# Kernel optimization log

Hardware: AMD Instinct MI355X
Metric: run time of the kernel (lower is better)

The kernel has to match this reference:

```python
import jax, jax.numpy as jnp
import numpy as np
from jax import lax

K = 3           # dynamic-filter kernel size
NUM_TYPES = 216 # Qstr*Qcohe*Qangle = 3*3*24
C = 64          # in/out channels
GROUP = 4


def _conv(x, w, groups=1):
    return lax.conv_general_dilated(
        x, w, window_strides=(1, 1), padding='SAME',
        dimension_numbers=('NCHW', 'OIHW', 'NCHW'),
        feature_group_count=groups)


def setup_inputs() -> dict:
    key = jax.random.key(0)
    ks = jax.random.split(key, 7)
    B, H, W = 1, 64, 64
    x = jax.random.normal(ks[0], (B, C, H, W), dtype=jnp.float32)
    buckets = jax.random.randint(ks[1], (B, H, W), 0, NUM_TYPES)
    # body1: grouped 3x3 conv (in=out=64, groups=4 -> in/group=16)
    w1 = jax.random.normal(ks[2], (C, C // GROUP, 3, 3), dtype=jnp.float32) * 0.05
    b1 = jax.random.normal(ks[3], (C,), dtype=jnp.float32) * 0.05
    # filter embedding: one flattened (out, in*K*K + bias) filter per bucket type
    emb = jax.random.normal(ks[4], (NUM_TYPES, C * (C * K * K + 1)), dtype=jnp.float32) * 0.1
    # body2: 1x1 conv
    w2 = jax.random.normal(ks[5], (C, C, 1, 1), dtype=jnp.float32) * 0.05
    b2 = jax.random.normal(ks[6], (C,), dtype=jnp.float32) * 0.05
    return {'x': x, 'buckets': buckets, 'w1': w1, 'b1': b1, 'emb': emb, 'w2': w2, 'b2': b2}


def reference(x, buckets, w1, b1, emb, w2, b2):
    B, Cin, H, W = x.shape
    Cout = w2.shape[0]
    ckk = emb.shape[1] // Cout - 1  # in*K*K
    # body1: grouped conv + ReLU
    h = jax.nn.relu(_conv(x, w1, groups=GROUP) + b1[None, :, None, None])
    # per-pixel bucket-indexed dynamic conv
    patches = lax.conv_general_dilated_patches(
        h, (K, K), (1, 1), 'SAME',
        dimension_numbers=('NCHW', 'OIHW', 'NCHW'))  # [B, Cin*K*K, H, W]
    f = emb[buckets].reshape(B, H, W, Cout, ckk + 1)   # gathered per-pixel filters
    out = jnp.einsum('bchw,bhwoc->bohw', patches, f[..., :-1])
    out = out + jnp.transpose(f[..., -1], (0, 3, 1, 2))  # per-pixel bias
    # body2: ReLU -> 1x1 conv
    out = _conv(jax.nn.relu(out), w2) + b2[None, :, None, None]
    # residual + ReLU
    return jax.nn.relu(out + x)
```

## Files before the change

kernel.cpp:

```cpp
#include <hip/hip_runtime.h>

#define NTYPES 216
#define NPIX   4096
#define KD     576
#define ROWLEN 577
#define NPC    32
#define PSTR   640

typedef __attribute__((ext_vector_type(8))) short short8;
typedef __attribute__((ext_vector_type(4))) float f32x4;
typedef __attribute__((ext_vector_type(4), aligned(4))) float f32x4u;
typedef __attribute__((ext_vector_type(8))) unsigned short u16x8;
typedef __attribute__((ext_vector_type(4))) unsigned short u16x4;

static __device__ __forceinline__ unsigned short f2bf(float f) {
    unsigned u = __builtin_bit_cast(unsigned, f);
    unsigned r = (u + 0x7FFFu + ((u >> 16) & 1u)) >> 16;
    return (unsigned short)r;
}

__global__ __launch_bounds__(256) void prep_kernel(
        const float* __restrict__ x, const float* __restrict__ w1,
        const float* __restrict__ b1, const int* __restrict__ buckets,
        unsigned short* __restrict__ hbf, int* __restrict__ offsets,
        int* __restrict__ sorted) {
    int tid = threadIdx.x;
    if (blockIdx.x == 256) {
        __shared__ int cnt[256];
        __shared__ int pre[256];
        cnt[tid] = 0;
        __syncthreads();
        for (int i = tid; i < NPIX; i += 256) atomicAdd(&cnt[buckets[i]], 1);
        __syncthreads();
        int v = cnt[tid];
        pre[tid] = v;
        __syncthreads();
        #pragma unroll
        for (int s = 1; s < 256; s <<= 1) {
            int add = (tid >= s) ? pre[tid - s] : 0;
            __syncthreads();
            pre[tid] += add;
            __syncthreads();
        }
        int excl = pre[tid] - v;
        if (tid <= NTYPES) offsets[tid] = excl;
        cnt[tid] = excl;
        __syncthreads();
        for (int i = tid; i < NPIX; i += 256) {
            int b = buckets[i];
            sorted[atomicAdd(&cnt[b], 1)] = i;
        }
        return;
    }
    int flat = blockIdx.x * 256 + tid;
    int x4 = flat & 15;
    int y  = (flat >> 4) & 63;
    int c  = flat >> 10;
    int g  = c >> 4;
    const float* wrow = w1 + c * 144;
    float o0, o1, o2, o3;
    o0 = o1 = o2 = o3 = b1[c];
    #pragma unroll
    for (int ci = 0; ci < 16; ++ci) {
        const float* xp = x + (g * 16 + ci) * 4096;
        #pragma unroll
        for (int dy = 0; dy < 3; ++dy) {
            int yy = y + dy - 1;
            if (yy < 0 || yy > 63) continue;
            const float* row = xp + yy * 64 + x4 * 4;
            f32x4 mm = *(const f32x4*)row;
            float xl = (x4 > 0)  ? row[-1] : 0.f;
            float xr = (x4 < 15) ? row[4]  : 0.f;
            float wa = wrow[ci * 9 + dy * 3 + 0];
            float wb = wrow[ci * 9 + dy * 3 + 1];
            float wc = wrow[ci * 9 + dy * 3 + 2];
            o0 = fmaf(wa, xl,    fmaf(wb, mm[0], fmaf(wc, mm[1], o0)));
            o1 = fmaf(wa, mm[0], fmaf(wb, mm[1], fmaf(wc, mm[2], o1)));
            o2 = fmaf(wa, mm[1], fmaf(wb, mm[2], fmaf(wc, mm[3], o2)));
            o3 = fmaf(wa, mm[2], fmaf(wb, mm[3], fmaf(wc, xr,    o3)));
        }
    }
    u16x4 r16;
    r16[0] = f2bf(fmaxf(o0, 0.f));
    r16[1] = f2bf(fmaxf(o1, 0.f));
    r16[2] = f2bf(fmaxf(o2, 0.f));
    r16[3] = f2bf(fmaxf(o3, 0.f));
    *(u16x4*)&hbf[flat * 4] = r16;
}

__global__ __launch_bounds__(512) void dyn_kernel(
        const unsigned short* __restrict__ hbf, const float* __restrict__ emb,
        const float* __restrict__ w2, const float* __restrict__ b2,
        const float* __restrict__ x, const int* __restrict__ offsets,
        const int* __restrict__ sorted, float* __restrict__ out) {

    __shared__ alignas(16) unsigned short Wl[64 * PSTR];
    __shared__ alignas(16) unsigned short Pl[NPC * PSTR];
    __shared__ alignas(16) unsigned short Dl[NPC * 72];
    __shared__ alignas(16) unsigned short w2l[64 * 72];
    __shared__ float bias_l[64];
    __shared__ int pixs[NPC];

    int t = blockIdx.x;
    int start = offsets[t];
    int n = offsets[t + 1] - start;
    if (n <= 0) return;

    int tid  = threadIdx.x;
    int lane = tid & 63;
    int wv   = tid >> 6;
    int m    = wv & 3;
    int ph   = wv >> 2;
    int ra   = lane & 15;
    int kg   = lane >> 4;

    const float* eb = emb + (size_t)t * 36928;

    #pragma unroll
    for (int it = 0; it < 9; ++it) {
        int u  = tid + it * 512;
        int r  = u / 72;
        int c0 = (u - r * 72) * 8;
        const float* src = eb + r * ROWLEN + c0;
        f32x4u a = *(const f32x4u*)src;
        f32x4u b = *(const f32x4u*)(src + 4);
        u16x8 v;
        #pragma unroll
        for (int j = 0; j < 4; ++j) { v[j] = f2bf(a[j]); v[j + 4] = f2bf(b[j]); }
        *(u16x8*)&Wl[r * PSTR + (r & 7) * 8 + c0] = v;
    }
    if (tid < 64) bias_l[tid] = eb[tid * ROWLEN + KD];

    {
        int o = tid >> 3, i8 = (tid & 7) * 8;
        const float* src = w2 + o * 64 + i8;
        u16x8 v;
        #pragma unroll
        for (int j = 0; j < 8; ++j) v[j] = f2bf(src[j]);
        *(u16x8*)&w2l[o * 72 + i8] = v;
    }
    __syncthreads();

    int rowW = m * 16 + ra;
    const unsigned short* pW = Wl + rowW * PSTR + (rowW & 7) * 8 + kg * 8;
    u16x8 Wr[9][2];
    #pragma unroll
    for (int ck = 0; ck < 9; ++ck) {
        Wr[ck][0] = *(const u16x8*)(pW + ck * 64);
        Wr[ck][1] = *(const u16x8*)(pW + ck * 64 + 32);
    }
    int ob0 = m * 16 + kg * 4;
    float bias0 = bias_l[ob0 + 0], bias1 = bias_l[ob0 + 1];
    float bias2 = bias_l[ob0 + 2], bias3 = bias_l[ob0 + 3];

    const unsigned short* pB = Pl + (ph * 16 + ra) * PSTR + (ra & 7) * 8 + kg * 8;

    int gp = tid >> 4;
    int gk = tid & 15;
    unsigned short* pdst = Pl + gp * PSTR + (gp & 7) * 8;

    for (int base = 0; base < n; base += NPC) {
        __syncthreads();
        if (tid < NPC) pixs[tid] = (base + tid < n) ? sorted[start + base + tid] : -1;
        __syncthreads();

        {
            int pixel = pixs[gp];
            int py = pixel >> 6, px = pixel & 63;
            #pragma unroll
            for (int pass = 0; pass < 9; ++pass) {
                int k0 = pass * 64 + gk * 4;
                u16x4 v;
                #pragma unroll
                for (int j = 0; j < 4; ++j) {
                    int k = k0 + j;
                    int cch = k / 9, r9 = k - cch * 9;
                    int dy = r9 / 3, dx = r9 - dy * 3;
                    unsigned short bits = 0;
                    if (pixel >= 0) {
                        int yy = py + dy - 1, xx = px + dx - 1;
                        if (yy >= 0 && yy < 64 && xx >= 0 && xx < 64)
                            bits = hbf[cch * 4096 + yy * 64 + xx];
                    }
                    v[j] = bits;
                }
                *(u16x4*)(pdst + k0) = v;
            }
        }
        __syncthreads();

        f32x4 acc = {0.f, 0.f, 0.f, 0.f};
        #pragma unroll
        for (int ck = 0; ck < 9; ++ck) {
            #pragma unroll
            for (int ks = 0; ks < 2; ++ks) {
                u16x8 bv = *(const u16x8*)(pB + ck * 64 + ks * 32);
                acc = __builtin_amdgcn_mfma_f32_16x16x32_bf16(
                          __builtin_bit_cast(short8, Wr[ck][ks]),
                          __builtin_bit_cast(short8, bv), acc, 0, 0, 0);
            }
        }

        {
            int pi = ph * 16 + ra;
            u16x4 dv;
            dv[0] = f2bf(fmaxf(acc[0] + bias0, 0.f));
            dv[1] = f2bf(fmaxf(acc[1] + bias1, 0.f));
            dv[2] = f2bf(fmaxf(acc[2] + bias2, 0.f));
            dv[3] = f2bf(fmaxf(acc[3] + bias3, 0.f));
            *(u16x4*)&Dl[pi * 72 + ob0] = dv;
        }
        __syncthreads();

        f32x4 acc2 = {0.f, 0.f, 0.f, 0.f};
        #pragma unroll
        for (int ks = 0; ks < 2; ++ks) {
            u16x8 a2  = *(const u16x8*)&w2l[(m * 16 + ra) * 72 + ks * 32 + kg * 8];
            u16x8 b2v = *(const u16x8*)&Dl[(ph * 16 + ra) * 72 + ks * 32 + kg * 8];
            acc2 = __builtin_amdgcn_mfma_f32_16x16x32_bf16(
                       __builtin_bit_cast(short8, a2),
                       __builtin_bit_cast(short8, b2v), acc2, 0, 0, 0);
        }

        {
            int pi = ph * 16 + ra;
            int pixel = pixs[pi];
            if (pixel >= 0) {
                #pragma unroll
                for (int j = 0; j < 4; ++j) {
                    int o = ob0 + j;
                    float v = acc2[j] + b2[o] + x[o * 4096 + pixel];
                    out[o * 4096 + pixel] = fmaxf(v, 0.f);
                }
            }
        }
    }
}

extern "C" void kernel_launch(void* const* d_in, const int* in_sizes, int n_in,
                              void* d_out, int out_size, void* d_ws, size_t ws_size,
                              hipStream_t stream) {
    const float* x       = (const float*)d_in[0];
    const int*   buckets = (const int*)d_in[1];
    const float* w1      = (const float*)d_in[2];
    const float* b1      = (const float*)d_in[3];
    const float* emb     = (const float*)d_in[4];
    const float* w2      = (const float*)d_in[5];
    const float* b2      = (const float*)d_in[6];
    float* out = (float*)d_out;

    char* ws = (char*)d_ws;
    unsigned short* hbf = (unsigned short*)ws;
    int*   offsets      = (int*)(ws + (1 << 20));
    int*   sorted       = (int*)(ws + (1 << 20) + 4096);

    prep_kernel<<<257, 256, 0, stream>>>(x, w1, b1, buckets, hbf, offsets, sorted);
    dyn_kernel<<<NTYPES, 512, 0, stream>>>(hbf, emb, w2, b2, x, offsets, sorted, out);
}
```

Before: 37.62 us.

## Fuse prep and dynamic-filter kernels into one cooperative launch with grid sync

The grouped-conv prep, the bucket sort and the dynamic per-bucket filter stage now run in a single cooperative kernel of 216 blocks, separated by a grid-wide sync. Each block issues its embedding-filter loads before doing prep work, so that global load latency overlaps the grouped conv and sort. This removes the second kernel launch and the gap between kernels. In exchange it adds cooperative-launch and grid-barrier overhead and puts more register pressure on the 512-thread prep path.

Result: slower. 114.6 us (+204.6%).

```diff
diff --git a/kernel.cpp b/kernel.cpp
--- a/kernel.cpp
+++ b/kernel.cpp
@@ -1,4 +1,7 @@
 #include <hip/hip_runtime.h>
+#include <hip/hip_cooperative_groups.h>
+
+namespace cg = cooperative_groups;
 
 #define NTYPES 216
 #define NPIX   4096
@@ -19,80 +22,13 @@
     return (unsigned short)r;
 }
 
-__global__ __launch_bounds__(256) void prep_kernel(
+__global__ __launch_bounds__(512) void fused_kernel(
         const float* __restrict__ x, const float* __restrict__ w1,
         const float* __restrict__ b1, const int* __restrict__ buckets,
+        const float* __restrict__ emb, const float* __restrict__ w2,
+        const float* __restrict__ b2,
         unsigned short* __restrict__ hbf, int* __restrict__ offsets,
-        int* __restrict__ sorted) {
-    int tid = threadIdx.x;
-    if (blockIdx.x == 256) {
-        __shared__ int cnt[256];
-        __shared__ int pre[256];
-        cnt[tid] = 0;
-        __syncthreads();
-        for (int i = tid; i < NPIX; i += 256) atomicAdd(&cnt[buckets[i]], 1);
-        __syncthreads();
-        int v = cnt[tid];
-        pre[tid] = v;
-        __syncthreads();
-        #pragma unroll
-        for (int s = 1; s < 256; s <<= 1) {
-            int add = (tid >= s) ? pre[tid - s] : 0;
-            __syncthreads();
-            pre[tid] += add;
-            __syncthreads();
-        }
-        int excl = pre[tid] - v;
-        if (tid <= NTYPES) offsets[tid] = excl;
-        cnt[tid] = excl;
-        __syncthreads();
-        for (int i = tid; i < NPIX; i += 256) {
-            int b = buckets[i];
-            sorted[atomicAdd(&cnt[b], 1)] = i;
-        }
-        return;
-    }
-    int flat = blockIdx.x * 256 + tid;
-    int x4 = flat & 15;
-    int y  = (flat >> 4) & 63;
-    int c  = flat >> 10;
-    int g  = c >> 4;
-    const float* wrow = w1 + c * 144;
-    float o0, o1, o2, o3;
-    o0 = o1 = o2 = o3 = b1[c];
-    #pragma unroll
-    for (int ci = 0; ci < 16; ++ci) {
-        const float* xp = x + (g * 16 + ci) * 4096;
-        #pragma unroll
-        for (int dy = 0; dy < 3; ++dy) {
-            int yy = y + dy - 1;
-            if (yy < 0 || yy > 63) continue;
-            const float* row = xp + yy * 64 + x4 * 4;
-            f32x4 mm = *(const f32x4*)row;
-            float xl = (x4 > 0)  ? row[-1] : 0.f;
-            float xr = (x4 < 15) ? row[4]  : 0.f;
-            float wa = wrow[ci * 9 + dy * 3 + 0];
-            float wb = wrow[ci * 9 + dy * 3 + 1];
-            float wc = wrow[ci * 9 + dy * 3 + 2];
-            o0 = fmaf(wa, xl,    fmaf(wb, mm[0], fmaf(wc, mm[1], o0)));
-            o1 = fmaf(wa, mm[0], fmaf(wb, mm[1], fmaf(wc, mm[2], o1)));
-            o2 = fmaf(wa, mm[1], fmaf(wb, mm[2], fmaf(wc, mm[3], o2)));
-            o3 = fmaf(wa, mm[2], fmaf(wb, mm[3], fmaf(wc, xr,    o3)));
-        }
-    }
-    u16x4 r16;
-    r16[0] = f2bf(fmaxf(o0, 0.f));
-    r16[1] = f2bf(fmaxf(o1, 0.f));
-    r16[2] = f2bf(fmaxf(o2, 0.f));
-    r16[3] = f2bf(fmaxf(o3, 0.f));
-    *(u16x4*)&hbf[flat * 4] = r16;
-}
-
-__global__ __launch_bounds__(512) void dyn_kernel(
-        const unsigned short* __restrict__ hbf, const float* __restrict__ emb,
-        const float* __restrict__ w2, const float* __restrict__ b2,
-        const float* __restrict__ x, const int* __restrict__ offsets,
-        const int* __restrict__ sorted, float* __restrict__ out) {
+        int* __restrict__ sorted, float* __restrict__ out) {
 
     __shared__ alignas(16) unsigned short Wl[64 * PSTR];
     __shared__ alignas(16) unsigned short Pl[NPC * PSTR];
@@ -100,137 +36,215 @@
     __shared__ alignas(16) unsigned short w2l[64 * 72];
     __shared__ float bias_l[64];
     __shared__ int pixs[NPC];
-
-    int t = blockIdx.x;
-    int start = offsets[t];
-    int n = offsets[t + 1] - start;
-    if (n <= 0) return;
-
-    int tid  = threadIdx.x;
-    int lane = tid & 63;
-    int wv   = tid >> 6;
-    int m    = wv & 3;
-    int ph   = wv >> 2;
-    int ra   = lane & 15;
-    int kg   = lane >> 4;
-
+    __shared__ int cnt[256];
+    __shared__ int pre[256];
+
+    int tid = threadIdx.x;
+    int t   = blockIdx.x;
     const float* eb = emb + (size_t)t * 36928;
 
+    f32x4u wa[9], wb[9];
     #pragma unroll
     for (int it = 0; it < 9; ++it) {
         int u  = tid + it * 512;
         int r  = u / 72;
         int c0 = (u - r * 72) * 8;
         const float* src = eb + r * ROWLEN + c0;
-        f32x4u a = *(const f32x4u*)src;
-        f32x4u b = *(const f32x4u*)(src + 4);
-        u16x8 v;
-        #pragma unroll
-        for (int j = 0; j < 4; ++j) { v[j] = f2bf(a[j]); v[j + 4] = f2bf(b[j]); }
-        *(u16x8*)&Wl[r * PSTR + (r & 7) * 8 + c0] = v;
-    }
-    if (tid < 64) bias_l[tid] = eb[tid * ROWLEN + KD];
+        wa[it] = *(const f32x4u*)src;
+        wb[it] = *(const f32x4u*)(src + 4);
+    }
+    float biasv = (tid < 64) ? eb[tid * ROWLEN + KD] : 0.f;
 
     {
         int o = tid >> 3, i8 = (tid & 7) * 8;
-        const float* src = w2 + o * 64 + i8;
+        const float* s2 = w2 + o * 64 + i8;
+        f32x4 q0 = *(const f32x4*)s2;
+        f32x4 q1 = *(const f32x4*)(s2 + 4);
         u16x8 v;
         #pragma unroll
-        for (int j = 0; j < 8; ++j) v[j] = f2bf(src[j]);
+        for (int j = 0; j < 4; ++j) { v[j] = f2bf(q0[j]); v[j + 4] = f2bf(q1[j]); }
         *(u16x8*)&w2l[o * 72 + i8] = v;
     }
-    __syncthreads();
-
-    int rowW = m * 16 + ra;
-    const unsigned short* pW = Wl + rowW * PSTR + (rowW & 7) * 8 + kg * 8;
-    u16x8 Wr[9][2];
+    if (tid < 64) bias_l[tid] = biasv;
+
+    if (blockIdx.x < 128) {
+        int flat = blockIdx.x * 512 + tid;
+        int x4 = flat & 15;
+        int y  = (flat >> 4) & 63;
+        int c  = flat >> 10;
+        int g  = c >> 4;
+        const float* wrow = w1 + c * 144;
+        float o0, o1, o2, o3;
+        o0 = o1 = o2 = o3 = b1[c];
+        #pragma unroll
+        for (int ci = 0; ci < 16; ++ci) {
+            const float* xp = x + (g * 16 + ci) * 4096;
+            #pragma unroll
+            for (int dy = 0; dy < 3; ++dy) {
+                int yy = y + dy - 1;
+                if (yy < 0 || yy > 63) continue;
+                const float* row = xp + yy * 64 + x4 * 4;
+                f32x4 mm = *(const f32x4*)row;
+                float xl = (x4 > 0)  ? row[-1] : 0.f;
+                float xr = (x4 < 15) ? row[4]  : 0.f;
+                float wwa = wrow[ci * 9 + dy * 3 + 0];
+                float wwb = wrow[ci * 9 + dy * 3 + 1];
+                float wwc = wrow[ci * 9 + dy * 3 + 2];
+                o0 = fmaf(wwa, xl,    fmaf(wwb, mm[0], fmaf(wwc, mm[1], o0)));
+                o1 = fmaf(wwa, mm[0], fmaf(wwb, mm[1], fmaf(wwc, mm[2], o1)));
+                o2 = fmaf(wwa, mm[1], fmaf(wwb, mm[2], fmaf(wwc, mm[3], o2)));
+                o3 = fmaf(wwa, mm[2], fmaf(wwb, mm[3], fmaf(wwc, xr,    o3)));
+            }
+        }
+        u16x4 r16;
+        r16[0] = f2bf(fmaxf(o0, 0.f));
+        r16[1] = f2bf(fmaxf(o1, 0.f));
+        r16[2] = f2bf(fmaxf(o2, 0.f));
+        r16[3] = f2bf(fmaxf(o3, 0.f));
+        *(u16x4*)&hbf[flat * 4] = r16;
+    } else if (blockIdx.x == 128) {
+        if (tid < 256) cnt[tid] = 0;
+        __syncthreads();
+        for (int i = tid; i < NPIX; i += 512) atomicAdd(&cnt[buckets[i]], 1);
+        __syncthreads();
+        int v = 0;
+        if (tid < 256) { v = cnt[tid]; pre[tid] = v; }
+        __syncthreads();
+        #pragma unroll
+        for (int s = 1; s < 256; s <<= 1) {
+            int add = (tid < 256 && tid >= s) ? pre[tid - s] : 0;
+            __syncthreads();
+            if (tid < 256) pre[tid] += add;
+            __syncthreads();
+        }
+        if (tid < 256) {
+            int excl = pre[tid] - v;
+            if (tid <= NTYPES) offsets[tid] = excl;
+            cnt[tid] = excl;
+        }
+        __syncthreads();
+        for (int i = tid; i < NPIX; i += 512) {
+            int b = buckets[i];
+            sorted[atomicAdd(&cnt[b], 1)] = i;
+        }
+    }
+
     #pragma unroll
-    for (int ck = 0; ck < 9; ++ck) {
-        Wr[ck][0] = *(const u16x8*)(pW + ck * 64);
-        Wr[ck][1] = *(const u16x8*)(pW + ck * 64 + 32);
-    }
-    int ob0 = m * 16 + kg * 4;
-    float bias0 = bias_l[ob0 + 0], bias1 = bias_l[ob0 + 1];
-    float bias2 = bias_l[ob0 + 2], bias3 = bias_l[ob0 + 3];
-
-    const unsigned short* pB = Pl + (ph * 16 + ra) * PSTR + (ra & 7) * 8 + kg * 8;
-
-    int gp = tid >> 4;
-    int gk = tid & 15;
-    unsigned short* pdst = Pl + gp * PSTR + (gp & 7) * 8;
-
-    for (int base = 0; base < n; base += NPC) {
-        __syncthreads();
-        if (tid < NPC) pixs[tid] = (base + tid < n) ? sorted[start + base + tid] : -1;
-        __syncthreads();
-
-        {
-            int pixel = pixs[gp];
-            int py = pixel >> 6, px = pixel & 63;
+    for (int it = 0; it < 9; ++it) {
+        int u  = tid + it * 512;
+        int r  = u / 72;
+        int c0 = (u - r * 72) * 8;
+        u16x8 v;
+        #pragma unroll
+        for (int j = 0; j < 4; ++j) { v[j] = f2bf(wa[it][j]); v[j + 4] = f2bf(wb[it][j]); }
+        *(u16x8*)&Wl[r * PSTR + (r & 7) * 8 + c0] = v;
+    }
+
+    __builtin_amdgcn_fence(__ATOMIC_RELEASE, "agent");
+    cg::this_grid().sync();
+    __builtin_amdgcn_fence(__ATOMIC_ACQUIRE, "agent");
+
+    int start = offsets[t];
+    int n = offsets[t + 1] - start;
+    if (n > 0) {
+        int lane = tid & 63;
+        int wv   = tid >> 6;
+        int m    = wv & 3;
+        int ph   = wv >> 2;
+        int ra   = lane & 15;
+        int kg   = lane >> 4;
+
+        int rowW = m * 16 + ra;
+        const unsigned short* pW = Wl + rowW * PSTR + (rowW & 7) * 8 + kg * 8;
+        u16x8 Wr[9][2];
+        #pragma unroll
+        for (int ck = 0; ck < 9; ++ck) {
+            Wr[ck][0] = *(const u16x8*)(pW + ck * 64);
+            Wr[ck][1] = *(const u16x8*)(pW + ck * 64 + 32);
+        }
+        int ob0 = m * 16 + kg * 4;
+        float bias0 = bias_l[ob0 + 0], bias1 = bias_l[ob0 + 1];
+        float bias2 = bias_l[ob0 + 2], bias3 = bias_l[ob0 + 3];
+
+        const unsigned short* pB = Pl + (ph * 16 + ra) * PSTR + (ra & 7) * 8 + kg * 8;
+
+        int gp = tid >> 4;
+        int gk = tid & 15;
+        unsigned short* pdst = Pl + gp * PSTR + (gp & 7) * 8;
+
+        for (int base = 0; base < n; base += NPC) {
+            __syncthreads();
+            if (tid < NPC) pixs[tid] = (base + tid < n) ? sorted[start + base + tid] : -1;
+            __syncthreads();
+
+            {
+                int pixel = pixs[gp];
+                int py = pixel >> 6, px = pixel & 63;
+                #pragma unroll
+                for (int pass = 0; pass < 9; ++pass) {
+                    int k0 = pass * 64 + gk * 4;
+                    u16x4 v;
+                    #pragma unroll
+                    for (int j = 0; j < 4; ++j) {
+                        int k = k0 + j;
+                        int cch = k / 9, r9 = k - cch * 9;
+                        int dy = r9 / 3, dx = r9 - dy * 3;
+                        unsigned short bits = 0;
+                        if (pixel >= 0) {
+                            int yy = py + dy - 1, xx = px + dx - 1;
+                            if (yy >= 0 && yy < 64 && xx >= 0 && xx < 64)
+                                bits = hbf[cch * 4096 + yy * 64 + xx];
+                        }
+                        v[j] = bits;
+                    }
+                    *(u16x4*)(pdst + k0) = v;
+                }
+            }
+            __syncthreads();
+
+            f32x4 acc = {0.f, 0.f, 0.f, 0.f};
             #pragma unroll
-            for (int pass = 0; pass < 9; ++pass) {
-                int k0 = pass * 64 + gk * 4;
-                u16x4 v;
+            for (int ck = 0; ck < 9; ++ck) {
                 #pragma unroll
-                for (int j = 0; j < 4; ++j) {
-                    int k = k0 + j;
-                    int cch = k / 9, r9 = k - cch * 9;
-                    int dy = r9 / 3, dx = r9 - dy * 3;
-                    unsigned short bits = 0;
-                    if (pixel >= 0) {
-                        int yy = py + dy - 1, xx = px + dx - 1;
-                        if (yy >= 0 && yy < 64 && xx >= 0 && xx < 64)
-                            bits = hbf[cch * 4096 + yy * 64 + xx];
-                    }
-                    v[j] = bits;
+                for (int ks = 0; ks < 2; ++ks) {
+                    u16x8 bv = *(const u16x8*)(pB + ck * 64 + ks * 32);
+                    acc = __builtin_amdgcn_mfma_f32_16x16x32_bf16(
+                              __builtin_bit_cast(short8, Wr[ck][ks]),
+                              __builtin_bit_cast(short8, bv), acc, 0, 0, 0);
                 }
-                *(u16x4*)(pdst + k0) = v;
-            }
-        }
-        __syncthreads();
-
-        f32x4 acc = {0.f, 0.f, 0.f, 0.f};
-        #pragma unroll
-        for (int ck = 0; ck < 9; ++ck) {
+            }
+
+            {
+                int pi = ph * 16 + ra;
+                u16x4 dv;
+                dv[0] = f2bf(fmaxf(acc[0] + bias0, 0.f));
+                dv[1] = f2bf(fmaxf(acc[1] + bias1, 0.f));
+                dv[2] = f2bf(fmaxf(acc[2] + bias2, 0.f));
+                dv[3] = f2bf(fmaxf(acc[3] + bias3, 0.f));
+                *(u16x4*)&Dl[pi * 72 + ob0] = dv;
+            }
+            __syncthreads();
+
+            f32x4 acc2 = {0.f, 0.f, 0.f, 0.f};
             #pragma unroll
             for (int ks = 0; ks < 2; ++ks) {
-                u16x8 bv = *(const u16x8*)(pB + ck * 64 + ks * 32);
-                acc = __builtin_amdgcn_mfma_f32_16x16x32_bf16(
-                          __builtin_bit_cast(short8, Wr[ck][ks]),
-                          __builtin_bit_cast(short8, bv), acc, 0, 0, 0);
-            }
-        }
-
-        {
-            int pi = ph * 16 + ra;
-            u16x4 dv;
-            dv[0] = f2bf(fmaxf(acc[0] + bias0, 0.f));
-            dv[1] = f2bf(fmaxf(acc[1] + bias1, 0.f));
-            dv[2] = f2bf(fmaxf(acc[2] + bias2, 0.f));
-            dv[3] = f2bf(fmaxf(acc[3] + bias3, 0.f));
-            *(u16x4*)&Dl[pi * 72 + ob0] = dv;
-        }
-        __syncthreads();
-
-        f32x4 acc2 = {0.f, 0.f, 0.f, 0.f};
-        #pragma unroll
-        for (int ks = 0; ks < 2; ++ks) {
-            u16x8 a2  = *(const u16x8*)&w2l[(m * 16 + ra) * 72 + ks * 32 + kg * 8];
-            u16x8 b2v = *(const u16x8*)&Dl[(ph * 16 + ra) * 72 + ks * 32 + kg * 8];
-            acc2 = __builtin_amdgcn_mfma_f32_16x16x32_bf16(
-                       __builtin_bit_cast(short8, a2),
-                       __builtin_bit_cast(short8, b2v), acc2, 0, 0, 0);
-        }
-
-        {
-            int pi = ph * 16 + ra;
-            int pixel = pixs[pi];
-            if (pixel >= 0) {
-                #pragma unroll
-                for (int j = 0; j < 4; ++j) {
-                    int o = ob0 + j;
-                    float v = acc2[j] + b2[o] + x[o * 4096 + pixel];
-                    out[o * 4096 + pixel] = fmaxf(v, 0.f);
+                u16x8 a2  = *(const u16x8*)&w2l[(m * 16 + ra) * 72 + ks * 32 + kg * 8];
+                u16x8 b2v = *(const u16x8*)&Dl[(ph * 16 + ra) * 72 + ks * 32 + kg * 8];
+                acc2 = __builtin_amdgcn_mfma_f32_16x16x32_bf16(
+                           __builtin_bit_cast(short8, a2),
+                           __builtin_bit_cast(short8, b2v), acc2, 0, 0, 0);
+            }
+
+            {
+                int pi = ph * 16 + ra;
+                int pixel = pixs[pi];
+                if (pixel >= 0) {
+                    #pragma unroll
+                    for (int j = 0; j < 4; ++j) {
+                        int o = ob0 + j;
+                        float v = acc2[j] + b2[o] + x[o * 4096 + pixel];
+                        out[o * 4096 + pixel] = fmaxf(v, 0.f);
+                    }
                 }
             }
         }
@@ -254,6 +268,11 @@
     int*   offsets      = (int*)(ws + (1 << 20));
     int*   sorted       = (int*)(ws + (1 << 20) + 4096);
 
-    prep_kernel<<<257, 256, 0, stream>>>(x, w1, b1, buckets, hbf, offsets, sorted);
-    dyn_kernel<<<NTYPES, 512, 0, stream>>>(hbf, emb, w2, b2, x, offsets, sorted, out);
+    void* args[] = {
+        (void*)&x, (void*)&w1, (void*)&b1, (void*)&buckets, (void*)&emb,
+        (void*)&w2, (void*)&b2, (void*)&hbf, (void*)&offsets, (void*)&sorted,
+        (void*)&out
+    };
+    hipLaunchCooperativeKernel((void*)fused_kernel, dim3(NTYPES), dim3(512),
+                               args, 0, stream);
 }
```

## Double pixel chunk to 64 and reuse filter LDS buffer for patches

Applied to the files above, without the earlier changes.

Once the per-bucket filter has been loaded into registers, its LDS buffer is reused to hold the patch tile. Each wave now computes two 16-pixel MFMA tiles per iteration, so 64 pixels are handled per chunk. This halves the number of chunk iterations and barrier rounds for buckets with more than 32 pixels and frees shared memory. With about 19 pixels per bucket on average, most blocks run a single chunk either way, and the larger chunk means more padded, zero-filled rows.

After: 59.36 us. +57.8%, slower.

```diff
diff --git a/kernel.cpp b/kernel.cpp
--- a/kernel.cpp
+++ b/kernel.cpp
@@ -4,7 +4,7 @@
 #define NPIX   4096
 #define KD     576
 #define ROWLEN 577
-#define NPC    32
+#define NPC    64
 #define PSTR   640
 
 typedef __attribute__((ext_vector_type(8))) short short8;
@@ -94,8 +94,7 @@
         const float* __restrict__ x, const int* __restrict__ offsets,
         const int* __restrict__ sorted, float* __restrict__ out) {
 
-    __shared__ alignas(16) unsigned short Wl[64 * PSTR];
-    __shared__ alignas(16) unsigned short Pl[NPC * PSTR];
+    __shared__ alignas(16) unsigned short WP[64 * PSTR];
     __shared__ alignas(16) unsigned short Dl[NPC * 72];
     __shared__ alignas(16) unsigned short w2l[64 * 72];
     __shared__ float bias_l[64];
@@ -110,7 +109,7 @@
     int lane = tid & 63;
     int wv   = tid >> 6;
     int m    = wv & 3;
-    int ph   = wv >> 2;
+    int ph2  = wv >> 2;
     int ra   = lane & 15;
     int kg   = lane >> 4;
 
@@ -127,7 +126,7 @@
         u16x8 v;
         #pragma unroll
         for (int j = 0; j < 4; ++j) { v[j] = f2bf(a[j]); v[j + 4] = f2bf(b[j]); }
-        *(u16x8*)&Wl[r * PSTR + (r & 7) * 8 + c0] = v;
+        *(u16x8*)&WP[r * PSTR + (r & 7) * 8 + c0] = v;
     }
     if (tid < 64) bias_l[tid] = eb[tid * ROWLEN + KD];
 
@@ -142,7 +141,7 @@
     __syncthreads();
 
     int rowW = m * 16 + ra;
-    const unsigned short* pW = Wl + rowW * PSTR + (rowW & 7) * 8 + kg * 8;
+    const unsigned short* pW = WP + rowW * PSTR + (rowW & 7) * 8 + kg * 8;
     u16x8 Wr[9][2];
     #pragma unroll
     for (int ck = 0; ck < 9; ++ck) {
@@ -153,11 +152,13 @@
     float bias0 = bias_l[ob0 + 0], bias1 = bias_l[ob0 + 1];
     float bias2 = bias_l[ob0 + 2], bias3 = bias_l[ob0 + 3];
 
-    const unsigned short* pB = Pl + (ph * 16 + ra) * PSTR + (ra & 7) * 8 + kg * 8;
-
-    int gp = tid >> 4;
-    int gk = tid & 15;
-    unsigned short* pdst = Pl + gp * PSTR + (gp & 7) * 8;
+    int q0 = ph2 * 2, q1 = ph2 * 2 + 1;
+    const unsigned short* pB0 = WP + (q0 * 16 + ra) * PSTR + (ra & 7) * 8 + kg * 8;
+    const unsigned short* pB1 = WP + (q1 * 16 + ra) * PSTR + (ra & 7) * 8 + kg * 8;
+
+    int gp = tid >> 3;
+    int gk = tid & 7;
+    unsigned short* pdst = WP + gp * PSTR + (gp & 7) * 8;
 
     for (int base = 0; base < n; base += NPC) {
         __syncthreads();
@@ -166,71 +167,99 @@
 
         {
             int pixel = pixs[gp];
-            int py = pixel >> 6, px = pixel & 63;
-            #pragma unroll
-            for (int pass = 0; pass < 9; ++pass) {
-                int k0 = pass * 64 + gk * 4;
-                u16x4 v;
-                #pragma unroll
-                for (int j = 0; j < 4; ++j) {
-                    int k = k0 + j;
-                    int cch = k / 9, r9 = k - cch * 9;
-                    int dy = r9 / 3, dx = r9 - dy * 3;
-                    unsigned short bits = 0;
-                    if (pixel >= 0) {
+            if (pixel >= 0) {
+                int py = pixel >> 6, px = pixel & 63;
+                #pragma unroll
+                for (int pass = 0; pass < 9; ++pass) {
+                    int k0 = pass * 64 + gk * 8;
+                    u16x8 v;
+                    #pragma unroll
+                    for (int j = 0; j < 8; ++j) {
+                        int k = k0 + j;
+                        int cch = k / 9, r9 = k - cch * 9;
+                        int dy = r9 / 3, dx = r9 - dy * 3;
+                        unsigned short bits = 0;
                         int yy = py + dy - 1, xx = px + dx - 1;
                         if (yy >= 0 && yy < 64 && xx >= 0 && xx < 64)
                             bits = hbf[cch * 4096 + yy * 64 + xx];
+                        v[j] = bits;
                     }
-                    v[j] = bits;
+                    *(u16x8*)(pdst + k0) = v;
                 }
-                *(u16x4*)(pdst + k0) = v;
-            }
-        }
-        __syncthreads();
-
-        f32x4 acc = {0.f, 0.f, 0.f, 0.f};
+            } else {
+                u16x8 z = {0, 0, 0, 0, 0, 0, 0, 0};
+                #pragma unroll
+                for (int pass = 0; pass < 9; ++pass)
+                    *(u16x8*)(pdst + pass * 64 + gk * 8) = z;
+            }
+        }
+        __syncthreads();
+
+        f32x4 acc0 = {0.f, 0.f, 0.f, 0.f};
+        f32x4 acc1 = {0.f, 0.f, 0.f, 0.f};
         #pragma unroll
         for (int ck = 0; ck < 9; ++ck) {
             #pragma unroll
             for (int ks = 0; ks < 2; ++ks) {
-                u16x8 bv = *(const u16x8*)(pB + ck * 64 + ks * 32);
-                acc = __builtin_amdgcn_mfma_f32_16x16x32_bf16(
+                u16x8 bv0 = *(const u16x8*)(pB0 + ck * 64 + ks * 32);
+                u16x8 bv1 = *(const u16x8*)(pB1 + ck * 64 + ks * 32);
+                acc0 = __builtin_amdgcn_mfma_f32_16x16x32_bf16(
                           __builtin_bit_cast(short8, Wr[ck][ks]),
-                          __builtin_bit_cast(short8, bv), acc, 0, 0, 0);
+                          __builtin_bit_cast(short8, bv0), acc0, 0, 0, 0);
+                acc1 = __builtin_amdgcn_mfma_f32_16x16x32_bf16(
+                          __builtin_bit_cast(short8, Wr[ck][ks]),
+                          __builtin_bit_cast(short8, bv1), acc1, 0, 0, 0);
             }
         }
 
         {
-            int pi = ph * 16 + ra;
-            u16x4 dv;
-            dv[0] = f2bf(fmaxf(acc[0] + bias0, 0.f));
-            dv[1] = f2bf(fmaxf(acc[1] + bias1, 0.f));
-            dv[2] = f2bf(fmaxf(acc[2] + bias2, 0.f));
-            dv[3] = f2bf(fmaxf(acc[3] + bias3, 0.f));
-            *(u16x4*)&Dl[pi * 72 + ob0] = dv;
-        }
-        __syncthreads();
-
-        f32x4 acc2 = {0.f, 0.f, 0.f, 0.f};
+            int pi0 = q0 * 16 + ra, pi1 = q1 * 16 + ra;
+            u16x4 dv0, dv1;
+            dv0[0] = f2bf(fmaxf(acc0[0] + bias0, 0.f));
+            dv0[1] = f2bf(fmaxf(acc0[1] + bias1, 0.f));
+            dv0[2] = f2bf(fmaxf(acc0[2] + bias2, 0.f));
+            dv0[3] = f2bf(fmaxf(acc0[3] + bias3, 0.f));
+            dv1[0] = f2bf(fmaxf(acc1[0] + bias0, 0.f));
+            dv1[1] = f2bf(fmaxf(acc1[1] + bias1, 0.f));
+            dv1[2] = f2bf(fmaxf(acc1[2] + bias2, 0.f));
+            dv1[3] = f2bf(fmaxf(acc1[3] + bias3, 0.f));
+            *(u16x4*)&Dl[pi0 * 72 + ob0] = dv0;
+            *(u16x4*)&Dl[pi1 * 72 + ob0] = dv1;
+        }
+        __syncthreads();
+
+        f32x4 acc2_0 = {0.f, 0.f, 0.f, 0.f};
+        f32x4 acc2_1 = {0.f, 0.f, 0.f, 0.f};
         #pragma unroll
         for (int ks = 0; ks < 2; ++ks) {
-            u16x8 a2  = *(const u16x8*)&w2l[(m * 16 + ra) * 72 + ks * 32 + kg * 8];
-            u16x8 b2v = *(const u16x8*)&Dl[(ph * 16 + ra) * 72 + ks * 32 + kg * 8];
-            acc2 = __builtin_amdgcn_mfma_f32_16x16x32_bf16(
-                       __builtin_bit_cast(short8, a2),
-                       __builtin_bit_cast(short8, b2v), acc2, 0, 0, 0);
+            u16x8 a2 = *(const u16x8*)&w2l[(m * 16 + ra) * 72 + ks * 32 + kg * 8];
+            u16x8 d0 = *(const u16x8*)&Dl[(q0 * 16 + ra) * 72 + ks * 32 + kg * 8];
+            u16x8 d1 = *(const u16x8*)&Dl[(q1 * 16 + ra) * 72 + ks * 32 + kg * 8];
+            acc2_0 = __builtin_amdgcn_mfma_f32_16x16x32_bf16(
+                         __builtin_bit_cast(short8, a2),
+                         __builtin_bit_cast(short8, d0), acc2_0, 0, 0, 0);
+            acc2_1 = __builtin_amdgcn_mfma_f32_16x16x32_bf16(
+                         __builtin_bit_cast(short8, a2),
+                         __builtin_bit_cast(short8, d1), acc2_1, 0, 0, 0);
         }
 
         {
-            int pi = ph * 16 + ra;
-            int pixel = pixs[pi];
-            if (pixel >= 0) {
+            int pix0 = pixs[q0 * 16 + ra];
+            int pix1 = pixs[q1 * 16 + ra];
+            if (pix0 >= 0) {
                 #pragma unroll
                 for (int j = 0; j < 4; ++j) {
                     int o = ob0 + j;
-                    float v = acc2[j] + b2[o] + x[o * 4096 + pixel];
-                    out[o * 4096 + pixel] = fmaxf(v, 0.f);
+                    float v = acc2_0[j] + b2[o] + x[o * 4096 + pix0];
+                    out[o * 4096 + pix0] = fmaxf(v, 0.f);
+                }
+            }
+            if (pix1 >= 0) {
+                #pragma unroll
+                for (int j = 0; j < 4; ++j) {
+                    int o = ob0 + j;
+                    float v = acc2_1[j] + b2[o] + x[o * 4096 + pix1];
+                    out[o * 4096 + pix1] = fmaxf(v, 0.f);
                 }
             }
         }
```
